# Performance work log

Hardware: AMD Instinct MI355X
Metric: run time of the kernel (lower is better)

Reference implementation:

```python
import jax, jax.numpy as jnp
import numpy as np

N_NODES = 50000
N_EDGES = 800000
N_GRAPHS = 64
IN_DIM = 128
HID4 = 256  # hidden_dim * 4
OUT_DIM = 256
EPS = 1e-5


def setup_inputs() -> dict:
    key = jax.random.key(0)
    ks = jax.random.split(key, 11)
    x = jax.random.normal(ks[0], (N_NODES, IN_DIM), jnp.float32)
    w = jax.random.uniform(ks[1], (N_EDGES,), jnp.float32)
    src = jax.random.randint(ks[2], (N_EDGES,), 0, N_NODES, dtype=jnp.int32)
    dst = jax.random.randint(ks[3], (N_EDGES,), 0, N_NODES, dtype=jnp.int32)
    graph_ids = jnp.sort(jax.random.randint(ks[4], (N_NODES,), 0, N_GRAPHS, dtype=jnp.int32))
    W1 = jax.random.normal(ks[5], (IN_DIM, HID4), jnp.float32) * 0.05
    Wfc = jax.random.normal(ks[6], (IN_DIM, HID4), jnp.float32) * 0.05
    gamma = jnp.ones((HID4,), jnp.float32)
    beta = jnp.zeros((HID4,), jnp.float32)
    W2 = jax.random.normal(ks[7], (2 * HID4, HID4), jnp.float32) * 0.05
    W3 = jax.random.normal(ks[8], (HID4, OUT_DIM), jnp.float32) * 0.05
    return {"x": x, "w": w, "W1": W1, "Wfc": Wfc, "gamma": gamma, "beta": beta,
            "W2": W2, "W3": W3, "src": src, "dst": dst, "graph_ids": graph_ids}


def _agg(h, src, dst, w, n):
    # edge-weighted SpMM: sum_{e: dst(e)=v} w_e * h[src(e)]
    return jax.ops.segment_sum(h[src] * w[:, None], dst, num_segments=n)


def _graph_conv(h, W, src, dst, w, out_norm, in_norm, n):
    # DGL GraphConv, norm='both', no bias, with edge_weight.
    h = h * out_norm  # D_out^{-1/2} on source side
    din, dout = W.shape
    if din > dout:  # DGL applies W first when it shrinks the width
        h = _agg(h @ W, src, dst, w, n)
    else:
        h = _agg(h, src, dst, w, n) @ W
    return h * in_norm  # D_in^{-1/2} on destination side


def _layer_norm(h, gamma, beta):
    mu = jnp.mean(h, axis=-1, keepdims=True)
    var = jnp.var(h, axis=-1, keepdims=True)
    return (h - mu) * jax.lax.rsqrt(var + EPS) * gamma + beta


def reference(x, w, W1, Wfc, gamma, beta, W2, W3, src, dst, graph_ids):
    n = x.shape[0]
    ones_e = jnp.ones(src.shape[0], jnp.float32)
    out_deg = jnp.maximum(jax.ops.segment_sum(ones_e, src, num_segments=n), 1.0)
    in_deg = jnp.maximum(jax.ops.segment_sum(ones_e, dst, num_segments=n), 1.0)
    out_norm = (out_deg ** -0.5)[:, None]
    in_norm = (in_deg ** -0.5)[:, None]

    x1 = jax.nn.relu(_graph_conv(x, W1, src, dst, w, out_norm, in_norm, n))
    f1 = jax.nn.relu(_layer_norm(x @ Wfc, gamma, beta))
    x1f1 = jnp.concatenate((x1, f1), axis=1)  # [N, 512]
    x2 = jax.nn.relu(_graph_conv(x1f1, W2, src, dst, w, out_norm, in_norm, n))
    x3 = jax.nn.relu(_graph_conv(x2, W3, src, dst, w, out_norm, in_norm, n))
    # dgl.sum_nodes: per-graph segment-sum readout
    readout = jax.ops.segment_sum(x3, graph_ids, num_segments=N_GRAPHS)
    return readout
```

## Files before the change

kernel.cpp:

```cpp
#include <hip/hip_runtime.h>

#define NN 50000
#define NE 800000
#define NG 64
#define EPSF 1e-5f

typedef __bf16 bf16x8 __attribute__((ext_vector_type(8)));
typedef float f32x4 __attribute__((ext_vector_type(4)));

#define AS1 __attribute__((address_space(1)))
#define AS3 __attribute__((address_space(3)))

__device__ __forceinline__ void gl_lds16(const unsigned short* g, unsigned short* l) {
#if __has_builtin(__builtin_amdgcn_global_load_lds)
  __builtin_amdgcn_global_load_lds((const AS1 void*)g, (AS3 void*)l, 16, 0, 0);
#else
  *(uint4*)l = *(const uint4*)g;
#endif
}

__device__ __forceinline__ unsigned short f2bf(float f) {
  unsigned u = __builtin_bit_cast(unsigned, f);
  u += 0x7fff + ((u >> 16) & 1);
  return (unsigned short)(u >> 16);
}
__device__ __forceinline__ float bf_lo(unsigned u) {
  return __builtin_bit_cast(float, u << 16);
}
__device__ __forceinline__ float bf_hi(unsigned u) {
  return __builtin_bit_cast(float, u & 0xffff0000u);
}

#define NB_H 64
#define EC   12500
#define HWORDS 12500
#define XB   1563
#define XTOT 1600000
#define WTB  256
__global__ __launch_bounds__(1024) void prep_kernel(
    const int* __restrict__ src, const int* __restrict__ dst,
    unsigned char* __restrict__ hout, unsigned char* __restrict__ hin,
    int* __restrict__ rank,
    const float* __restrict__ x, unsigned short* __restrict__ xb,
    const float* __restrict__ W1, const float* __restrict__ Wfc,
    const float* __restrict__ W2, const float* __restrict__ W3,
    unsigned short* __restrict__ W1t, unsigned short* __restrict__ Wfct,
    unsigned short* __restrict__ W2t, unsigned short* __restrict__ W3t) {
  __shared__ unsigned hist[HWORDS];
  int b = blockIdx.x;
  int tid = threadIdx.x;
  if (b < NB_H) {
    int e0 = b * EC;
#pragma unroll
    for (int ph = 0; ph < 2; ph++) {
      const int* key = ph ? src : dst;
      unsigned char* gh = (ph ? hout : hin) + (size_t)b * NN;
      for (int i = tid; i < HWORDS; i += 1024) hist[i] = 0u;
      __syncthreads();
      for (int i = tid; i < EC; i += 1024) {
        int k = key[e0 + i];
        int sh = (k & 3) << 3;
        unsigned old = atomicAdd(&hist[k >> 2], 1u << sh);
        if (ph == 0) rank[e0 + i] = (int)((old >> sh) & 0xffu);
      }
      __syncthreads();
      unsigned* gw = (unsigned*)gh;
      for (int i = tid; i < HWORDS; i += 1024) gw[i] = hist[i];
      __syncthreads();
    }
  } else if (b < NB_H + XB) {
    int i = (b - NB_H) * 1024 + tid;
    if (i < XTOT) {
      float4 v = ((const float4*)x)[i];
      uint2 pk;
      pk.x = (unsigned)f2bf(v.x) | ((unsigned)f2bf(v.y) << 16);
      pk.y = (unsigned)f2bf(v.z) | ((unsigned)f2bf(v.w) << 16);
      ((uint2*)xb)[i] = pk;
    }
  } else {
    int i = (b - NB_H - XB) * 1024 + tid;
    const float* W; unsigned short* Wt; int K, local;
    if (i < 32768)       { W = W1;  Wt = W1t;  K = 128; local = i; }
    else if (i < 65536)  { W = Wfc; Wt = Wfct; K = 128; local = i - 32768; }
    else if (i < 196608) { W = W2;  Wt = W2t;  K = 512; local = i - 65536; }
    else                 { W = W3;  Wt = W3t;  K = 256; local = i - 196608; }
    int n = local / K, k = local - n * K;
    Wt[local] = f2bf(W[(size_t)k * 256 + n]);
  }
}

__global__ void norms_scan1(const unsigned char* __restrict__ hout,
                            unsigned char* __restrict__ hin,
                            int* __restrict__ din,
                            float* __restrict__ onorm, float* __restrict__ inorm,
                            int* __restrict__ bsum, int n) {
  int i = blockIdx.x * 256 + threadIdx.x;
  int d = 0;
  if (i < n) {
    int a = 0;
    for (int b = 0; b < NB_H; b++) a += hout[(size_t)b * NN + i];
    int run = 0;
    for (int b = 0; b < NB_H; b++) {
      int t = hin[(size_t)b * NN + i];
      hin[(size_t)b * NN + i] = (unsigned char)run;
      run += t;
    }
    d = run;
    din[i] = run;
    onorm[i] = rsqrtf((float)(a > 1 ? a : 1));
    inorm[i] = rsqrtf((float)(d > 1 ? d : 1));
  }
  int v = d;
#pragma unroll
  for (int off = 32; off > 0; off >>= 1) v += __shfl_down(v, off);
  __shared__ int ws[4];
  int wave = threadIdx.x >> 6, lane = threadIdx.x & 63;
  if (lane == 0) ws[wave] = v;
  __syncthreads();
  if (threadIdx.x == 0) bsum[blockIdx.x] = ws[0] + ws[1] + ws[2] + ws[3];
}

__global__ void scan3_kernel(const int* __restrict__ din, const int* __restrict__ bsum,
                             int* __restrict__ rp, int n, int nb) {
  int t = threadIdx.x;
  int lane = t & 63, wave = t >> 6;
  int bj = (t < nb) ? bsum[t] : 0;
  int pre = (t < (int)blockIdx.x) ? bj : 0;
  int p = pre, q = bj;
#pragma unroll
  for (int off = 32; off > 0; off >>= 1) {
    p += __shfl_down(p, off);
    q += __shfl_down(q, off);
  }
  __shared__ int red[8];
  __shared__ int baseS, totS;
  if (lane == 0) { red[wave] = p; red[4 + wave] = q; }
  __syncthreads();
  if (t == 0) {
    baseS = red[0] + red[1] + red[2] + red[3];
    totS  = red[4] + red[5] + red[6] + red[7];
  }
  __syncthreads();
  int i = blockIdx.x * 256 + t;
  int v = (i < n) ? din[i] : 0;
  __shared__ int tmp[256];
  tmp[t] = v;
  __syncthreads();
  for (int off = 1; off < 256; off <<= 1) {
    int x = (t >= off) ? tmp[t - off] : 0;
    __syncthreads();
    tmp[t] += x;
    __syncthreads();
  }
  if (i < n) rp[i] = tmp[t] - v + baseS;
  if (blockIdx.x == gridDim.x - 1 && t == 0) rp[n] = totS;
}

__global__ void fill_kernel(const int* __restrict__ src, const int* __restrict__ dst,
                            const float* __restrict__ w, const float* __restrict__ onorm,
                            const float* __restrict__ inorm,
                            const int* __restrict__ rp, const int* __restrict__ rank,
                            const unsigned char* __restrict__ binBase,
                            uint2* __restrict__ edge, int E) {
  int e = blockIdx.x * 256 + threadIdx.x;
  if (e < E) {
    int d = dst[e], s = src[e];
    int b = e / EC;
    int pos = rp[d] + (int)binBase[(size_t)b * NN + d] + rank[e];
    float wv = w[e] * onorm[s] * inorm[d];
    edge[pos] = make_uint2((unsigned)s, __builtin_bit_cast(unsigned, wv));
  }
}

template <int RELU, int NU>
__global__ __launch_bounds__(64) void spmm_bf16(
    const unsigned short* __restrict__ feat, int ldf,
    const int* __restrict__ rp, const uint2* __restrict__ edge,
    unsigned short* __restrict__ out, int ldo) {
  int v = blockIdx.x;
  int t = threadIdx.x;
  int beg = rp[v], end = rp[v + 1];
  float acc[2 * NU];
#pragma unroll
  for (int i = 0; i < 2 * NU; i++) acc[i] = 0.f;
  const unsigned short* base = feat + t * (2 * NU);
  int e = beg;
  for (; e + 8 <= end; e += 8) {
    int s[8]; float ww[8];
#pragma unroll
    for (int k = 0; k < 8; k++) {
      uint2 q = edge[e + k];
      s[k] = (int)q.x;
      ww[k] = __builtin_bit_cast(float, q.y);
    }
    unsigned u[8][NU];
#pragma unroll
    for (int k = 0; k < 8; k++) {
      const unsigned* pr = (const unsigned*)&base[(size_t)s[k] * ldf];
      if (NU == 2) { uint2 q = *(const uint2*)pr; u[k][0] = q.x; u[k][NU - 1] = q.y; }
      else u[k][0] = pr[0];
    }
#pragma unroll
    for (int k = 0; k < 8; k++)
#pragma unroll
      for (int j = 0; j < NU; j++) {
        acc[2 * j]     += ww[k] * bf_lo(u[k][j]);
        acc[2 * j + 1] += ww[k] * bf_hi(u[k][j]);
      }
  }
  for (; e < end; e++) {
    uint2 qe = edge[e];
    float w0 = __builtin_bit_cast(float, qe.y);
    const unsigned* pr = (const unsigned*)&base[(size_t)qe.x * ldf];
    unsigned u[NU];
    if (NU == 2) { uint2 q = *(const uint2*)pr; u[0] = q.x; u[NU - 1] = q.y; }
    else u[0] = pr[0];
#pragma unroll
    for (int j = 0; j < NU; j++) {
      acc[2 * j]     += w0 * bf_lo(u[j]);
      acc[2 * j + 1] += w0 * bf_hi(u[j]);
    }
  }
  unsigned o[NU];
#pragma unroll
  for (int j = 0; j < NU; j++) {
    float a = acc[2 * j], b = acc[2 * j + 1];
    if (RELU) { a = fmaxf(a, 0.f); b = fmaxf(b, 0.f); }
    o[j] = (unsigned)f2bf(a) | ((unsigned)f2bf(b) << 16);
  }
  unsigned* po = (unsigned*)&out[(size_t)v * ldo + t * (2 * NU)];
  if (NU == 2) *(uint2*)po = make_uint2(o[0], o[NU - 1]);
  else po[0] = o[0];
}

__device__ __forceinline__ void gemm_core(
    const unsigned short* __restrict__ A, int lda,
    const unsigned short* __restrict__ Bt, int K, int M,
    int bm, int bn, int relu,
    unsigned short (*As)[8192], unsigned short (*Bs)[8192],
    f32x4 (&acc)[4][4]) {
  const int tid = threadIdx.x;
  const int lane = tid & 63;
  const int m0 = bm * 128;
  const int n0 = bn * 128;

#pragma unroll
  for (int i = 0; i < 4; i++)
#pragma unroll
    for (int j = 0; j < 4; j++) acc[i][j] = (f32x4){0.f, 0.f, 0.f, 0.f};

  const unsigned short* pa[4];
  const unsigned short* pb[4];
#pragma unroll
  for (int i = 0; i < 4; i++) {
    int ch = i * 256 + tid;
    int sub = ch >> 6, sl = ch & 63;
    int mi = sub >> 1, kk = sub & 1;
    int row = mi * 16 + (sl & 15);
    int kc = kk * 32 + (sl >> 4) * 8;
    int gm = m0 + row; if (gm >= M) gm = M - 1;
    pa[i] = A + (size_t)gm * lda + kc;
    int gn = n0 + row;
    pb[i] = Bt + (size_t)gn * K + kc;
  }

  const int NT = K >> 6;
#pragma unroll
  for (int i = 0; i < 4; i++) {
    int ch8 = (i * 256 + tid) * 8;
    gl_lds16(pa[i], &As[0][ch8]);
    gl_lds16(pb[i], &Bs[0][ch8]);
  }
  __syncthreads();

  const int wv = tid >> 6;
  const int wm = wv >> 1, wn = wv & 1;
  int cur = 0;
  for (int t = 0; t < NT; t++) {
    if (t + 1 < NT) {
      int nk = (t + 1) << 6;
#pragma unroll
      for (int i = 0; i < 4; i++) {
        int ch8 = (i * 256 + tid) * 8;
        gl_lds16(pa[i] + nk, &As[cur ^ 1][ch8]);
        gl_lds16(pb[i] + nk, &Bs[cur ^ 1][ch8]);
      }
    }
#pragma unroll
    for (int kk = 0; kk < 2; kk++) {
      bf16x8 af[4], bfr[4];
#pragma unroll
      for (int i = 0; i < 4; i++)
        af[i] = *(const bf16x8*)&As[cur][((wm * 4 + i) * 2 + kk) * 512 + lane * 8];
#pragma unroll
      for (int j = 0; j < 4; j++)
        bfr[j] = *(const bf16x8*)&Bs[cur][((wn * 4 + j) * 2 + kk) * 512 + lane * 8];
#pragma unroll
      for (int i = 0; i < 4; i++)
#pragma unroll
        for (int j = 0; j < 4; j++)
          acc[i][j] = __builtin_amdgcn_mfma_f32_16x16x32_bf16(af[i], bfr[j], acc[i][j], 0, 0, 0);
    }
    __syncthreads();
    cur ^= 1;
  }
  if (relu) {
#pragma unroll
    for (int i = 0; i < 4; i++)
#pragma unroll
      for (int j = 0; j < 4; j++)
#pragma unroll
        for (int r = 0; r < 4; r++) acc[i][j][r] = fmaxf(acc[i][j][r], 0.f);
  }
}

__device__ __forceinline__ void gemm_store(
    const f32x4 (&acc)[4][4], unsigned short* __restrict__ C, int ldc,
    int col_off, int M, int bm, int bn) {
  const int tid = threadIdx.x;
  const int lane = tid & 63;
  const int wv = tid >> 6;
  const int wm = wv >> 1, wn = wv & 1;
  const int q = lane >> 4, r16 = lane & 15;
  const int m0 = bm * 128, n0 = bn * 128;
#pragma unroll
  for (int i = 0; i < 4; i++) {
    int rbase = m0 + wm * 64 + i * 16 + q * 4;
#pragma unroll
    for (int r = 0; r < 4; r++) {
      int gm = rbase + r;
      if (gm >= M) continue;
#pragma unroll
      for (int j = 0; j < 4; j++) {
        int gn = col_off + n0 + wn * 64 + j * 16 + r16;
        C[(size_t)gm * ldc + gn] = f2bf(acc[i][j][r]);
      }
    }
  }
}

__device__ __forceinline__ void fcln_body(
    const unsigned short* __restrict__ A, const unsigned short* __restrict__ Bt,
    const float* __restrict__ gamma, const float* __restrict__ beta,
    unsigned short* __restrict__ C, int M, unsigned short* lds) {
  const int tid = threadIdx.x;
  const int lane = tid & 63;
  const int w = tid >> 6;
  const int q = lane >> 4, r16 = lane & 15;
  const int m0 = blockIdx.x * 64;
  unsigned short* As = lds;
  unsigned short* Bs = lds + 8192;

#pragma unroll
  for (int i = 0; i < 4; i++) {
    int ch = i * 256 + tid;
    int st = ch >> 6, sl = ch & 63;
    int mi = st >> 2, kk = st & 3;
    int gm = m0 + mi * 16 + (sl & 15); if (gm >= M) gm = M - 1;
    int k = kk * 32 + (sl >> 4) * 8;
    gl_lds16(A + (size_t)gm * 128 + k, &As[ch * 8]);
  }
#pragma unroll
  for (int i = 0; i < 16; i++) {
    int ch = i * 256 + tid;
    int st = ch >> 6, sl = ch & 63;
    int ns = st >> 2, kk = st & 3;
    int n = ns * 16 + (sl & 15);
    int k = kk * 32 + (sl >> 4) * 8;
    gl_lds16(Bt + (size_t)n * 128 + k, &Bs[ch * 8]);
  }
  __syncthreads();

  f32x4 acc[4][4];
#pragma unroll
  for (int i = 0; i < 4; i++)
#pragma unroll
    for (int j = 0; j < 4; j++) acc[i][j] = (f32x4){0.f, 0.f, 0.f, 0.f};

#pragma unroll
  for (int kk = 0; kk < 4; kk++) {
    bf16x8 af[4], bfr[4];
#pragma unroll
    for (int i = 0; i < 4; i++)
      af[i] = *(const bf16x8*)&As[(i * 4 + kk) * 512 + lane * 8];
#pragma unroll
    for (int j = 0; j < 4; j++)
      bfr[j] = *(const bf16x8*)&Bs[((w * 4 + j) * 4 + kk) * 512 + lane * 8];
#pragma unroll
    for (int i = 0; i < 4; i++)
#pragma unroll
      for (int j = 0; j < 4; j++)
        acc[i][j] = __builtin_amdgcn_mfma_f32_16x16x32_bf16(af[i], bfr[j], acc[i][j], 0, 0, 0);
  }
  __syncthreads();

  float* fws = (float*)lds;
  float* fwq = fws + 256;
  float* fmean = fwq + 256;
  float* frs = fmean + 64;

#pragma unroll
  for (int i = 0; i < 4; i++)
#pragma unroll
    for (int r = 0; r < 4; r++) {
      float s  = acc[i][0][r] + acc[i][1][r] + acc[i][2][r] + acc[i][3][r];
      float q2 = acc[i][0][r] * acc[i][0][r] + acc[i][1][r] * acc[i][1][r] +
                 acc[i][2][r] * acc[i][2][r] + acc[i][3][r] * acc[i][3][r];
#pragma unroll
      for (int off = 8; off > 0; off >>= 1) {
        s  += __shfl_down(s, off, 16);
        q2 += __shfl_down(q2, off, 16);
      }
      if (r16 == 0) {
        int row = i * 16 + q * 4 + r;
        fws[w * 64 + row] = s;
        fwq[w * 64 + row] = q2;
      }
    }
  __syncthreads();
  if (tid < 64) {
    float S = fws[tid] + fws[64 + tid] + fws[128 + tid] + fws[192 + tid];
    float Q = fwq[tid] + fwq[64 + tid] + fwq[128 + tid] + fwq[192 + tid];
    float mean = S * (1.f / 256.f);
    float var = Q * (1.f / 256.f) - mean * mean;
    fmean[tid] = mean;
    frs[tid] = rsqrtf(var + EPSF);
  }
  __syncthreads();

  float g4[4], b4[4];
#pragma unroll
  for (int j = 0; j < 4; j++) {
    int c = w * 64 + j * 16 + r16;
    g4[j] = gamma[c];
    b4[j] = beta[c];
  }
#pragma unroll
  for (int i = 0; i < 4; i++)
#pragma unroll
    for (int r = 0; r < 4; r++) {
      int row = i * 16 + q * 4 + r;
      int gm = m0 + row;
      if (gm >= M) continue;
      float mean = fmean[row], rs = frs[row];
#pragma unroll
      for (int j = 0; j < 4; j++) {
        int c = w * 64 + j * 16 + r16;
        float y = (acc[i][j][r] - mean) * rs * g4[j] + b4[j];
        C[(size_t)gm * 512 + 256 + c] = f2bf(fmaxf(y, 0.f));
      }
    }
}

__global__ __launch_bounds__(256) void g12f_kernel(
    const unsigned short* __restrict__ A0, const unsigned short* __restrict__ B0,
    const unsigned short* __restrict__ A1, const unsigned short* __restrict__ B1,
    const float* __restrict__ gamma, const float* __restrict__ beta,
    unsigned short* __restrict__ C, int M) {
  __shared__ unsigned short lds[40960];
  if (blockIdx.z == 0) {
    f32x4 acc[4][4];
    int bm = blockIdx.x >> 1, bn = blockIdx.x & 1;
    gemm_core(A0, 128, B0, 128, M, bm, bn, 1,
              (unsigned short (*)[8192])lds,
              (unsigned short (*)[8192])(lds + 16384), acc);
    gemm_store(acc, C, 512, 0, M, bm, bn);
  } else {
    fcln_body(A1, B1, gamma, beta, C, M, lds);
  }
}

__global__ __launch_bounds__(256) void gemm_kernel(
    const unsigned short* __restrict__ A, int lda,
    const unsigned short* __restrict__ Bt, int K,
    unsigned short* __restrict__ C, int ldc, int M, int relu) {
  __shared__ unsigned short As[2][8192];
  __shared__ unsigned short Bs[2][8192];
  f32x4 acc[4][4];
  gemm_core(A, lda, Bt, K, M, blockIdx.x, blockIdx.y, relu, As, Bs, acc);
  gemm_store(acc, C, ldc, 0, M, blockIdx.x, blockIdx.y);
}

__global__ __launch_bounds__(256) void gemm_ro2(
    const unsigned short* __restrict__ A,
    const unsigned short* __restrict__ Bt,
    const int* __restrict__ gid, float* __restrict__ part, int M) {
  __shared__ float red[4][256];
  const int tid = threadIdx.x;
  const int l = tid & 63;
  const int w = tid >> 6;
  const int v0 = blockIdx.x * 64;
  const int vw = v0 + w * 16;

  for (int i = tid; i < 1024; i += 256) ((float*)red)[i] = 0.f;
  __syncthreads();

  const int r16 = l & 15, q = l >> 4;
  int arow = vw + r16; if (arow >= M) arow = M - 1;
  const unsigned short* pa = A + (size_t)arow * 256 + q * 8;
  bf16x8 af[8];
#pragma unroll
  for (int kt = 0; kt < 8; kt++)
    af[kt] = *(const bf16x8*)&pa[kt * 32];

  int g0 = gid[v0];
  int slot[4];
#pragma unroll
  for (int j = 0; j < 4; j++) {
    int gm = vw + q * 4 + j;
    slot[j] = (gm < M) ? gid[gm] - g0 : -1;
  }
  bool uni = (slot[0] == slot[3]);

  const unsigned short* pb0 = Bt + (size_t)r16 * 256 + q * 8;
#pragma unroll 4
  for (int nt = 0; nt < 16; nt++) {
    const unsigned short* pb = pb0 + (size_t)(nt * 16) * 256;
    f32x4 acc = (f32x4){0.f, 0.f, 0.f, 0.f};
#pragma unroll
    for (int kt = 0; kt < 8; kt++) {
      bf16x8 bf = *(const bf16x8*)&pb[kt * 32];
      acc = __builtin_amdgcn_mfma_f32_16x16x32_bf16(af[kt], bf, acc, 0, 0, 0);
    }
    int col = nt * 16 + r16;
    if (uni) {
      if ((unsigned)slot[0] < 4u) {
        float s = fmaxf(acc[0], 0.f) + fmaxf(acc[1], 0.f) +
                  fmaxf(acc[2], 0.f) + fmaxf(acc[3], 0.f);
        atomicAdd(&red[slot[0]][col], s);
      }
    } else {
#pragma unroll
      for (int j = 0; j < 4; j++) {
        float vv = fmaxf(acc[j], 0.f);
        int sl = slot[j];
        if ((unsigned)sl < 4u && vv != 0.f) atomicAdd(&red[sl][col], vv);
      }
    }
  }
  __syncthreads();
  float* pp = part + (size_t)blockIdx.x * 1024;
  for (int i = tid; i < 1024; i += 256) pp[i] = ((float*)red)[i];
}

__global__ void readout_reduce(const float* __restrict__ part,
                               const int* __restrict__ gid,
                               float* __restrict__ out, int n) {
  int g = blockIdx.x;
  int c = threadIdx.x;
  int lo = 0, hi = n;
  while (lo < hi) { int mid = (lo + hi) >> 1; if (gid[mid] < g) lo = mid + 1; else hi = mid; }
  int s = lo;
  lo = s; hi = n;
  while (lo < hi) { int mid = (lo + hi) >> 1; if (gid[mid] < g + 1) lo = mid + 1; else hi = mid; }
  int e = lo;
  float acc = 0.f;
  if (s < e) {
    int b0 = s >> 6, b1 = (e - 1) >> 6;
    for (int b = b0; b <= b1; b++) {
      int sl = g - gid[b * 64];
      if ((unsigned)sl < 4u)
        acc += part[(size_t)b * 1024 + sl * 256 + c];
    }
  }
  out[g * 256 + c] = acc;
}


extern "C" void kernel_launch(void* const* d_in, const int* in_sizes, int n_in,
                              void* d_out, int out_size, void* d_ws, size_t ws_size,
                              hipStream_t stream) {
  const float* x     = (const float*)d_in[0];
  const float* w     = (const float*)d_in[1];
  const float* W1    = (const float*)d_in[2];
  const float* Wfc   = (const float*)d_in[3];
  const float* gamma = (const float*)d_in[4];
  const float* beta  = (const float*)d_in[5];
  const float* W2    = (const float*)d_in[6];
  const float* W3    = (const float*)d_in[7];
  const int*   src   = (const int*)d_in[8];
  const int*   dst   = (const int*)d_in[9];
  const int*   gid   = (const int*)d_in[10];
  float* out = (float*)d_out;

  const int N = NN, E = NE;

  char* p = (char*)d_ws;
  auto alloc = [&](size_t bytes) {
    char* r = p;
    p += (bytes + 255) & ~(size_t)255;
    return r;
  };
  unsigned char* hout = (unsigned char*)alloc((size_t)NB_H * N);
  unsigned char* hin  = (unsigned char*)alloc((size_t)NB_H * N);
  int*   din     = (int*)alloc((size_t)N * 4);
  float* onorm   = (float*)alloc((size_t)N * 4);
  float* inorm   = (float*)alloc((size_t)N * 4);
  int*   row_ptr = (int*)alloc((size_t)(N + 1) * 4);
  int*   bsum    = (int*)alloc(256 * 4);
  int*   rank    = (int*)alloc((size_t)E * 4);
  uint2* edge    = (uint2*)alloc((size_t)E * 8);
  float* part    = (float*)alloc((size_t)782 * 4 * 256 * 4);
  unsigned short* xb    = (unsigned short*)alloc((size_t)N * 128 * 2);
  unsigned short* aggX  = (unsigned short*)alloc((size_t)N * 128 * 2);
  unsigned short* x1f1  = (unsigned short*)alloc((size_t)N * 512 * 2);
  unsigned short* y2    = (unsigned short*)alloc((size_t)N * 256 * 2);
  unsigned short* x2    = (unsigned short*)alloc((size_t)N * 256 * 2);
  unsigned short* aggx2 = (unsigned short*)alloc((size_t)N * 256 * 2);
  unsigned short* W1t   = (unsigned short*)alloc((size_t)256 * 128 * 2);
  unsigned short* Wfct  = (unsigned short*)alloc((size_t)256 * 128 * 2);
  unsigned short* W2t   = (unsigned short*)alloc((size_t)256 * 512 * 2);
  unsigned short* W3t   = (unsigned short*)alloc((size_t)256 * 256 * 2);

  const int nbS = (N + 255) / 256;

  prep_kernel<<<NB_H + XB + WTB, 1024, 0, stream>>>(src, dst, hout, hin, rank,
                                                    x, xb, W1, Wfc, W2, W3,
                                                    W1t, Wfct, W2t, W3t);
  norms_scan1<<<nbS, 256, 0, stream>>>(hout, hin, din, onorm, inorm, bsum, N);
  scan3_kernel<<<nbS, 256, 0, stream>>>(din, bsum, row_ptr, N, nbS);
  fill_kernel<<<(E + 255) / 256, 256, 0, stream>>>(src, dst, w, onorm, inorm, row_ptr,
                                                   rank, hin, edge, E);

  dim3 ggrid((N + 127) / 128, 2);

  spmm_bf16<0, 1><<<N, 64, 0, stream>>>(xb, 128, row_ptr, edge, aggX, 128);
  g12f_kernel<<<dim3(782, 1, 2), 256, 0, stream>>>(aggX, W1t, xb, Wfct, gamma, beta, x1f1, N);
  gemm_kernel<<<ggrid, 256, 0, stream>>>(x1f1, 512, W2t, 512, y2, 256, N, 0);
  spmm_bf16<1, 2><<<N, 64, 0, stream>>>(y2, 256, row_ptr, edge, x2, 256);
  spmm_bf16<0, 2><<<N, 64, 0, stream>>>(x2, 256, row_ptr, edge, aggx2, 256);
  gemm_ro2<<<782, 256, 0, stream>>>(aggx2, W3t, gid, part, N);
  readout_reduce<<<NG, 256, 0, stream>>>(part, gid, out, N);
}
```

Measured before the change: 415.1 us.

## Split final GEMM-readout over column tiles and stage operands through LDS

The fused layer-3 GEMM plus readout kernel now launches a 782x4 grid, so each block handles 64 output columns instead of all 256. A and B tiles are loaded into LDS with async global-to-LDS copies instead of direct per-lane global loads. The partial-sum layout and the readout reduction indexing change to match the new per-column-tile partials. This raises parallelism and makes B loads coalesced, at the cost of loading the A tile four times and dropping the uniform-graph fast path for the atomics.

```diff
diff --git a/kernel.cpp b/kernel.cpp
--- a/kernel.cpp
+++ b/kernel.cpp
@@ -481,28 +481,42 @@
   gemm_store(acc, C, ldc, 0, M, blockIdx.x, blockIdx.y);
 }
 
-__global__ __launch_bounds__(256) void gemm_ro2(
+__global__ __launch_bounds__(256) void gemm_ro3(
     const unsigned short* __restrict__ A,
     const unsigned short* __restrict__ Bt,
     const int* __restrict__ gid, float* __restrict__ part, int M) {
-  __shared__ float red[4][256];
+  __shared__ unsigned short As[32 * 512];
+  __shared__ unsigned short Bs[32 * 512];
+  __shared__ float red[4][64];
   const int tid = threadIdx.x;
   const int l = tid & 63;
   const int w = tid >> 6;
   const int v0 = blockIdx.x * 64;
+  const int n0 = blockIdx.y * 64;
+
+#pragma unroll
+  for (int i = 0; i < 8; i++) {
+    int ch = i * 256 + tid;
+    int st = ch >> 6, sl = ch & 63;
+    int rt = st >> 3, kt = st & 7;
+    int gm = v0 + rt * 16 + (sl & 15); if (gm >= M) gm = M - 1;
+    int k = kt * 32 + (sl >> 4) * 8;
+    gl_lds16(A + (size_t)gm * 256 + k, &As[ch * 8]);
+  }
+#pragma unroll
+  for (int i = 0; i < 8; i++) {
+    int ch = i * 256 + tid;
+    int st = ch >> 6, sl = ch & 63;
+    int ct = st >> 3, kt = st & 7;
+    int row = n0 + ct * 16 + (sl & 15);
+    int k = kt * 32 + (sl >> 4) * 8;
+    gl_lds16(Bt + (size_t)row * 256 + k, &Bs[ch * 8]);
+  }
+  for (int i = tid; i < 256; i += 256) ((float*)red)[i] = 0.f;
+  __syncthreads();
+
+  const int r16 = l & 15, q = l >> 4;
   const int vw = v0 + w * 16;
-
-  for (int i = tid; i < 1024; i += 256) ((float*)red)[i] = 0.f;
-  __syncthreads();
-
-  const int r16 = l & 15, q = l >> 4;
-  int arow = vw + r16; if (arow >= M) arow = M - 1;
-  const unsigned short* pa = A + (size_t)arow * 256 + q * 8;
-  bf16x8 af[8];
-#pragma unroll
-  for (int kt = 0; kt < 8; kt++)
-    af[kt] = *(const bf16x8*)&pa[kt * 32];
-
   int g0 = gid[v0];
   int slot[4];
 #pragma unroll
@@ -510,37 +524,31 @@
     int gm = vw + q * 4 + j;
     slot[j] = (gm < M) ? gid[gm] - g0 : -1;
   }
-  bool uni = (slot[0] == slot[3]);
-
-  const unsigned short* pb0 = Bt + (size_t)r16 * 256 + q * 8;
-#pragma unroll 4
-  for (int nt = 0; nt < 16; nt++) {
-    const unsigned short* pb = pb0 + (size_t)(nt * 16) * 256;
+
+  bf16x8 af[8];
+#pragma unroll
+  for (int kt = 0; kt < 8; kt++)
+    af[kt] = *(const bf16x8*)&As[(w * 8 + kt) * 512 + l * 8];
+
+#pragma unroll
+  for (int ct = 0; ct < 4; ct++) {
     f32x4 acc = (f32x4){0.f, 0.f, 0.f, 0.f};
 #pragma unroll
     for (int kt = 0; kt < 8; kt++) {
-      bf16x8 bf = *(const bf16x8*)&pb[kt * 32];
+      bf16x8 bf = *(const bf16x8*)&Bs[(ct * 8 + kt) * 512 + l * 8];
       acc = __builtin_amdgcn_mfma_f32_16x16x32_bf16(af[kt], bf, acc, 0, 0, 0);
     }
-    int col = nt * 16 + r16;
-    if (uni) {
-      if ((unsigned)slot[0] < 4u) {
-        float s = fmaxf(acc[0], 0.f) + fmaxf(acc[1], 0.f) +
-                  fmaxf(acc[2], 0.f) + fmaxf(acc[3], 0.f);
-        atomicAdd(&red[slot[0]][col], s);
-      }
-    } else {
-#pragma unroll
-      for (int j = 0; j < 4; j++) {
-        float vv = fmaxf(acc[j], 0.f);
-        int sl = slot[j];
-        if ((unsigned)sl < 4u && vv != 0.f) atomicAdd(&red[sl][col], vv);
-      }
-    }
-  }
-  __syncthreads();
-  float* pp = part + (size_t)blockIdx.x * 1024;
-  for (int i = tid; i < 1024; i += 256) pp[i] = ((float*)red)[i];
+    int col = ct * 16 + r16;
+#pragma unroll
+    for (int j = 0; j < 4; j++) {
+      float vv = fmaxf(acc[j], 0.f);
+      int sl = slot[j];
+      if ((unsigned)sl < 4u && vv != 0.f) atomicAdd(&red[sl][col], vv);
+    }
+  }
+  __syncthreads();
+  float* pp = part + ((size_t)(blockIdx.x * 4 + blockIdx.y) * 4) * 64;
+  for (int i = tid; i < 256; i += 256) pp[i] = ((float*)red)[i];
 }
 
 __global__ void readout_reduce(const float* __restrict__ part,
@@ -556,11 +564,12 @@
   int e = lo;
   float acc = 0.f;
   if (s < e) {
+    int cb = c >> 6, cc = c & 63;
     int b0 = s >> 6, b1 = (e - 1) >> 6;
     for (int b = b0; b <= b1; b++) {
       int sl = g - gid[b * 64];
       if ((unsigned)sl < 4u)
-        acc += part[(size_t)b * 1024 + sl * 256 + c];
+        acc += part[(((size_t)b * 4 + cb) * 4 + sl) * 64 + cc];
     }
   }
   out[g * 256 + c] = acc;
@@ -600,7 +609,7 @@
   int*   bsum    = (int*)alloc(256 * 4);
   int*   rank    = (int*)alloc((size_t)E * 4);
   uint2* edge    = (uint2*)alloc((size_t)E * 8);
-  float* part    = (float*)alloc((size_t)782 * 4 * 256 * 4);
+  float* part    = (float*)alloc((size_t)782 * 4 * 4 * 64 * 4);
   unsigned short* xb    = (unsigned short*)alloc((size_t)N * 128 * 2);
   unsigned short* aggX  = (unsigned short*)alloc((size_t)N * 128 * 2);
   unsigned short* x1f1  = (unsigned short*)alloc((size_t)N * 512 * 2);
@@ -629,6 +638,6 @@
   gemm_kernel<<<ggrid, 256, 0, stream>>>(x1f1, 512, W2t, 512, y2, 256, N, 0);
   spmm_bf16<1, 2><<<N, 64, 0, stream>>>(y2, 256, row_ptr, edge, x2, 256);
   spmm_bf16<0, 2><<<N, 64, 0, stream>>>(x2, 256, row_ptr, edge, aggx2, 256);
-  gemm_ro2<<<782, 256, 0, stream>>>(aggx2, W3t, gid, part, N);
+  gemm_ro3<<<dim3(782, 4), 256, 0, stream>>>(aggx2, W3t, gid, part, N);
   readout_reduce<<<NG, 256, 0, stream>>>(part, gid, out, N);
 }
```

Measured after the change: 427.7 us. 1.03x slower.
